# Kernel tuning notes

Hardware: AMD Instinct MI355X
Metric: run time of the kernel (lower is better)

Reference implementation:

```python
import jax, jax.numpy as jnp
import numpy as np

B = 512      # batch
H = 64       # latent_dim == GRU hidden size
F = 32       # n_features
S = 2048     # seq_len
NEG_SLOPE = 0.01  # nn.LeakyReLU default


def setup_inputs() -> dict:
    key = jax.random.key(0)
    ks = jax.random.split(key, 14)

    def p(k, shape, scale=0.1):
        return jax.random.normal(k, shape, dtype=jnp.float32) * scale

    return {
        "noise": jax.random.normal(ks[0], (B, H), dtype=jnp.float32),
        # GRU forward direction (layer 0): weight_ih_l0, weight_hh_l0, biases
        "W_ih_f": p(ks[1], (3 * H, H)),
        "W_hh_f": p(ks[2], (3 * H, H)),
        "b_ih_f": p(ks[3], (3 * H,)),
        "b_hh_f": p(ks[4], (3 * H,)),
        # GRU backward direction (layer 0 reverse)
        "W_ih_b": p(ks[5], (3 * H, H)),
        "W_hh_b": p(ks[6], (3 * H, H)),
        "b_ih_b": p(ks[7], (3 * H,)),
        "b_hh_b": p(ks[8], (3 * H,)),
        # latent_linear: Linear(2H -> H)
        "W_lat": p(ks[9], (H, 2 * H)),
        "b_lat": p(ks[10], (H,)),
        # output_linear: Linear(H -> F)
        "W_out": p(ks[11], (F, H)),
        "b_out": p(ks[12], (F,)),
    }


def _leaky(x):
    return jnp.where(x >= 0, x, NEG_SLOPE * x)


def _gru_cell(x, h, W_ih, W_hh, b_ih, b_hh):
    # PyTorch GRU cell: gates ordered (r, z, n)
    gi = x @ W_ih.T + b_ih          # (B, 3H)
    gh = h @ W_hh.T + b_hh          # (B, 3H)
    i_r, i_z, i_n = jnp.split(gi, 3, axis=-1)
    h_r, h_z, h_n = jnp.split(gh, 3, axis=-1)
    r = jax.nn.sigmoid(i_r + h_r)
    z = jax.nn.sigmoid(i_z + h_z)
    n = jnp.tanh(i_n + r * h_n)
    return (1.0 - z) * n + z * h


def reference(noise, W_ih_f, W_hh_f, b_ih_f, b_hh_f,
              W_ih_b, W_hh_b, b_ih_b, b_hh_b,
              W_lat, b_lat, W_out, b_out):
    # hidden_state = noise.repeat((D*n_layers,1,1)) -> both directions start at noise
    batch = noise.shape[0]

    def step(carry, _):
        x, hf, hb = carry
        # GRU on a length-1 sequence: each direction does one cell update;
        # output timestep = concat(fwd_out, bwd_out)
        hf2 = _gru_cell(x, hf, W_ih_f, W_hh_f, b_ih_f, b_hh_f)
        hb2 = _gru_cell(x, hb, W_ih_b, W_hh_b, b_ih_b, b_hh_b)
        out = jnp.concatenate([hf2, hb2], axis=-1)        # (B, 2H)
        lat = _leaky(out @ W_lat.T + b_lat)               # (B, H)
        return (lat, hf2, hb2), lat

    x0 = jnp.zeros((batch, H), dtype=noise.dtype)
    _, ys = jax.lax.scan(step, (x0, noise, noise), None, length=S)
    seq = jnp.transpose(ys, (1, 0, 2))   # (B, S, H)
    seq = _leaky(seq)                    # second LeakyReLU as in the original
    out = jax.nn.sigmoid(seq @ W_out.T + b_out)  # (B, S, F)
    return out
```

## Files before the change

kernel.cpp:

```cpp
#include <hip/hip_runtime.h>
#include <hip/hip_bf16.h>


#define NBATCH 512
#define NH 64
#define NS 2048
#define NF 32
#define MROW 16
#define LDH 72

typedef short s16x8 __attribute__((ext_vector_type(8)));
typedef float f32x4 __attribute__((ext_vector_type(4)));

#define MFMA(a, b, c) __builtin_amdgcn_mfma_f32_16x16x32_bf16((a), (b), (c), 0, 0, 0)

#define NLOG2E  (-1.4426950408889634f)
#define N2LOG2E (-2.8853900817779268f)

__device__ __forceinline__ short f2bf(float f) {
    return (short)((__float_as_uint(f) + 0x8000u) >> 16);
}

__device__ __forceinline__ f32x4 v_exp2(f32x4 a) {
    f32x4 r;
#pragma unroll
    for (int i = 0; i < 4; ++i) r[i] = __builtin_amdgcn_exp2f(a[i]);
    return r;
}

__device__ __forceinline__ f32x4 v_rcp(f32x4 a) {
    f32x4 r;
#pragma unroll
    for (int i = 0; i < 4; ++i) r[i] = __builtin_amdgcn_rcpf(a[i]);
    return r;
}

__device__ __forceinline__ f32x4 v_lk(f32x4 a) {
    f32x4 b = a * 0.01f;
    f32x4 r;
#pragma unroll
    for (int i = 0; i < 4; ++i) r[i] = fmaxf(a[i], b[i]);
    return r;
}

__device__ __forceinline__ f32x4 v_sigm(f32x4 a) {
    return v_rcp(v_exp2(a * NLOG2E) + 1.0f);
}

__device__ __forceinline__ int2 pk4bf(f32x4 v) {
    union { __hip_bfloat162 b; int i; } lo, hi;
    float2 a; a.x = v[0]; a.y = v[1];
    float2 b; b.x = v[2]; b.y = v[3];
    lo.b = __float22bfloat162_rn(a);
    hi.b = __float22bfloat162_rn(b);
    int2 r; r.x = lo.i; r.y = hi.i;
    return r;
}

__device__ __forceinline__ s16x8 bfragW(const float* __restrict__ W, int ldk,
                                        int row, int kf, int quad) {
    const float* p = W + (size_t)row * ldk + kf * 32 + quad * 8;
    s16x8 r;
#pragma unroll
    for (int i = 0; i < 8; ++i) r[i] = f2bf(p[i]);
    return r;
}

__device__ __forceinline__ f32x4 bias4(const float* __restrict__ p) {
    const float4 v = *(const float4*)p;
    f32x4 r = {v.x, v.y, v.z, v.w};
    return r;
}

__global__ __launch_bounds__(1024)
void grugan_kernel(const float* __restrict__ noise,
                   const float* __restrict__ Wihf, const float* __restrict__ Whhf,
                   const float* __restrict__ bihf, const float* __restrict__ bhhf,
                   const float* __restrict__ Wihb, const float* __restrict__ Whhb,
                   const float* __restrict__ bihb, const float* __restrict__ bhhb,
                   const float* __restrict__ Wlat, const float* __restrict__ blat,
                   const float* __restrict__ Wout, const float* __restrict__ bout,
                   float* __restrict__ out)
{
    __shared__ __align__(16) short Xs[2][MROW][LDH];
    __shared__ __align__(16) short X2s[2][MROW][LDH];
    __shared__ __align__(16) short Hs[2][2][MROW][LDH];

    const int tid  = threadIdx.x;
    const int wave = tid >> 6;
    const int lane = tid & 63;
    const int n    = lane & 15;
    const int quad = lane >> 4;
    const int row0 = blockIdx.x * MROW;

    for (int idx = tid; idx < MROW * LDH; idx += 1024) (&Xs[0][0][0])[idx] = 0;
    f32x4 hreg = {0.f, 0.f, 0.f, 0.f};
    const int gdir = wave >> 2;
    const int gjq  = (wave & 3) * 16 + quad * 4;
    if (wave < 8) {
        const float4 nz = *(const float4*)&noise[(size_t)(row0 + n) * NH + gjq];
        hreg[0] = nz.x; hreg[1] = nz.y; hreg[2] = nz.z; hreg[3] = nz.w;
        *(int2*)&Hs[0][gdir][n][gjq] = pk4bf(hreg);
    }
    __syncthreads();

    if (wave < 8) {
        const int dir  = gdir;
        const int cb   = wave & 3;
        const int jrow = cb * 16 + n;
        const int jq   = gjq;
        const float* Wih = dir ? Wihb : Wihf;
        const float* Whh = dir ? Whhb : Whhf;
        const float* bih = dir ? bihb : bihf;
        const float* bhh = dir ? bhhb : bhhf;

        s16x8 wir0 = bfragW(Wih, NH,   0 + jrow, 0, quad);
        s16x8 wir1 = bfragW(Wih, NH,   0 + jrow, 1, quad);
        s16x8 wiz0 = bfragW(Wih, NH,  64 + jrow, 0, quad);
        s16x8 wiz1 = bfragW(Wih, NH,  64 + jrow, 1, quad);
        s16x8 win0 = bfragW(Wih, NH, 128 + jrow, 0, quad);
        s16x8 win1 = bfragW(Wih, NH, 128 + jrow, 1, quad);
        s16x8 whr0 = bfragW(Whh, NH,   0 + jrow, 0, quad);
        s16x8 whr1 = bfragW(Whh, NH,   0 + jrow, 1, quad);
        s16x8 whz0 = bfragW(Whh, NH,  64 + jrow, 0, quad);
        s16x8 whz1 = bfragW(Whh, NH,  64 + jrow, 1, quad);
        s16x8 whn0 = bfragW(Whh, NH, 128 + jrow, 0, quad);
        s16x8 whn1 = bfragW(Whh, NH, 128 + jrow, 1, quad);
        f32x4 initR, initZ;
        {
            f32x4 a = bias4(&bih[jq]),      b = bias4(&bhh[jq]);
            initR = a + b;
            f32x4 c = bias4(&bih[64 + jq]), d = bias4(&bhh[64 + jq]);
            initZ = c + d;
        }
        const f32x4 initN1 = bias4(&bih[128 + jq]);
        const f32x4 initN2 = bias4(&bhh[128 + jq]);

        f32x4 accR, accZ, accN2;
        {
            s16x8 ha0 = *(const s16x8*)&Hs[0][dir][n][quad * 8];
            s16x8 ha1 = *(const s16x8*)&Hs[0][dir][n][32 + quad * 8];
            accR  = MFMA(whr0, ha0, initR);  accR  = MFMA(whr1, ha1, accR);
            accZ  = MFMA(whz0, ha0, initZ);  accZ  = MFMA(whz1, ha1, accZ);
            accN2 = MFMA(whn0, ha0, initN2); accN2 = MFMA(whn1, ha1, accN2);
        }

#define GSTEP(HB) do {                                                          \
        s16x8 xa0 = *(const s16x8*)&Xs[HB][n][quad * 8];                        \
        s16x8 xa1 = *(const s16x8*)&Xs[HB][n][32 + quad * 8];                   \
        accR = MFMA(wir0, xa0, accR);   accR = MFMA(wir1, xa1, accR);           \
        accZ = MFMA(wiz0, xa0, accZ);   accZ = MFMA(wiz1, xa1, accZ);           \
        f32x4 accN1 = MFMA(win0, xa0, initN1);                                  \
        accN1 = MFMA(win1, xa1, accN1);                                         \
        f32x4 eR = v_exp2(accR * NLOG2E);                                       \
        f32x4 rr = v_rcp(eR + 1.0f);                                            \
        f32x4 u  = accN1 + rr * accN2;                                          \
        f32x4 eU = v_exp2(u * N2LOG2E);                                         \
        f32x4 eZ = v_exp2(accZ * NLOG2E);                                       \
        f32x4 numer = (eZ + hreg) + eU * (hreg - eZ);                           \
        f32x4 denom = (eU + 1.0f) * (eZ + 1.0f);                                \
        hreg = numer * v_rcp(denom);                                            \
        *(int2*)&Hs[(HB) ^ 1][dir][n][jq] = pk4bf(hreg);                        \
        __syncthreads();                                \
        {                                                                       \
            s16x8 ha0 = *(const s16x8*)&Hs[(HB) ^ 1][dir][n][quad * 8];         \
            s16x8 ha1 = *(const s16x8*)&Hs[(HB) ^ 1][dir][n][32 + quad * 8];    \
            accR  = MFMA(whr0, ha0, initR);  accR  = MFMA(whr1, ha1, accR);     \
            accZ  = MFMA(whz0, ha0, initZ);  accZ  = MFMA(whz1, ha1, accZ);     \
            accN2 = MFMA(whn0, ha0, initN2); accN2 = MFMA(whn1, ha1, accN2);    \
        }                                                                       \
        __syncthreads();                                \
    } while (0)

        for (int t = 0; t < NS; t += 2) {
            GSTEP(0);
            GSTEP(1);
        }
#undef GSTEP
    } else if (wave < 12) {
        const int lt = wave & 3;
        const int nq = lt * 16 + quad * 4;
        s16x8 wl0 = bfragW(Wlat, 2 * NH, lt * 16 + n, 0, quad);
        s16x8 wl1 = bfragW(Wlat, 2 * NH, lt * 16 + n, 1, quad);
        s16x8 wl2 = bfragW(Wlat, 2 * NH, lt * 16 + n, 2, quad);
        s16x8 wl3 = bfragW(Wlat, 2 * NH, lt * 16 + n, 3, quad);
        const f32x4 initL = bias4(&blat[lt * 16 + quad * 4]);

#define LSTEP(HB) do {                                                          \
        __syncthreads();                                \
        s16x8 fa0 = *(const s16x8*)&Hs[(HB) ^ 1][0][n][quad * 8];               \
        s16x8 fa1 = *(const s16x8*)&Hs[(HB) ^ 1][0][n][32 + quad * 8];          \
        s16x8 ba0 = *(const s16x8*)&Hs[(HB) ^ 1][1][n][quad * 8];               \
        s16x8 ba1 = *(const s16x8*)&Hs[(HB) ^ 1][1][n][32 + quad * 8];          \
        f32x4 lac = MFMA(wl0, fa0, initL);                                      \
        lac = MFMA(wl1, fa1, lac);                                              \
        lac = MFMA(wl2, ba0, lac);                                              \
        lac = MFMA(wl3, ba1, lac);                                              \
        f32x4 la = v_lk(lac);                                                   \
        *(int2*)&Xs[(HB) ^ 1][n][nq]  = pk4bf(la);                              \
        *(int2*)&X2s[(HB) ^ 1][n][nq] = pk4bf(v_lk(la));                        \
        __syncthreads();                                \
    } while (0)

        for (int t = 0; t < NS; t += 2) {
            LSTEP(0);
            LSTEP(1);
        }
#undef LSTEP
    } else if (wave < 14) {
        const int f0 = (wave & 1) * 16;
        s16x8 wo0 = bfragW(Wout, NH, f0 + n, 0, quad);
        s16x8 wo1 = bfragW(Wout, NH, f0 + n, 1, quad);
        const f32x4 initO = bias4(&bout[f0 + quad * 4]);
        float* const orow = out + (size_t)(row0 + n) * (NS * NF) + f0 + quad * 4;
        f32x4 yv = {0.f, 0.f, 0.f, 0.f};

#define OSTEP(HB, T) do {                                                       \
        if ((T) >= 2)                                                           \
            *(f32x4*)(orow + (size_t)((T) - 2) * NF) = yv;                      \
        __syncthreads();                                                \
        if ((T) >= 1) {                                                         \
            s16x8 p0 = *(const s16x8*)&X2s[HB][n][quad * 8];                    \
            s16x8 p1 = *(const s16x8*)&X2s[HB][n][32 + quad * 8];               \
            f32x4 po = MFMA(wo0, p0, initO);                                    \
            po = MFMA(wo1, p1, po);                                             \
            yv = v_sigm(po);                                                    \
        }                                                                       \
        __syncthreads();                                                \
    } while (0)

        for (int t = 0; t < NS; t += 2) {
            OSTEP(0, t);
            OSTEP(1, t + 1);
        }
#undef OSTEP

        *(f32x4*)(orow + (size_t)(NS - 2) * NF) = yv;
        s16x8 p0 = *(const s16x8*)&X2s[0][n][quad * 8];
        s16x8 p1 = *(const s16x8*)&X2s[0][n][32 + quad * 8];
        f32x4 po = MFMA(wo0, p0, initO);
        po = MFMA(wo1, p1, po);
        *(f32x4*)(orow + (size_t)(NS - 1) * NF) = v_sigm(po);
    } else {
#pragma unroll 1
        for (int i = 0; i < 2 * NS; ++i) __syncthreads();
    }
}

extern "C" void kernel_launch(void* const* d_in, const int* in_sizes, int n_in,
                              void* d_out, int out_size, void* d_ws, size_t ws_size,
                              hipStream_t stream) {
    const float* noise = (const float*)d_in[0];
    const float* Wihf  = (const float*)d_in[1];
    const float* Whhf  = (const float*)d_in[2];
    const float* bihf  = (const float*)d_in[3];
    const float* bhhf  = (const float*)d_in[4];
    const float* Wihb  = (const float*)d_in[5];
    const float* Whhb  = (const float*)d_in[6];
    const float* bihb  = (const float*)d_in[7];
    const float* bhhb  = (const float*)d_in[8];
    const float* Wlat  = (const float*)d_in[9];
    const float* blat  = (const float*)d_in[10];
    const float* Wout  = (const float*)d_in[11];
    const float* bout  = (const float*)d_in[12];

    grugan_kernel<<<dim3(NBATCH / MROW), dim3(1024), 0, stream>>>(
        noise, Wihf, Whhf, bihf, bhhf, Wihb, Whhb, bihb, bhhb,
        Wlat, blat, Wout, bout, (float*)d_out);
}
```

Before: 1.613 ms.

## Merge output waves into latent waves and use non-draining raw barriers

The output projection moves into the two low latent waves, so the separate output waves and the idle barrier-only waves are dropped and the block shrinks from 1024 to 768 threads. The latent/output waves now use a raw s_barrier, and an s_barrier preceded only by an LDS wait, in place of __syncthreads. This keeps outstanding global stores of the output from stalling each per-timestep barrier. The latent MFMA chain is also split into two independent accumulators to shorten its dependency. The risk is a memory-ordering hazard if the hand-written barriers do not match the waits the compiler would otherwise insert, and the latent waves now sit longer on the serial critical path.

```diff
diff --git a/kernel.cpp b/kernel.cpp
--- a/kernel.cpp
+++ b/kernel.cpp
@@ -16,6 +16,14 @@
 
 #define NLOG2E  (-1.4426950408889634f)
 #define N2LOG2E (-2.8853900817779268f)
+
+__device__ __forceinline__ void bar_nodrain() {
+    asm volatile("s_barrier" ::: "memory");
+}
+
+__device__ __forceinline__ void bar_lgkm() {
+    asm volatile("s_waitcnt lgkmcnt(0)\n\ts_barrier" ::: "memory");
+}
 
 __device__ __forceinline__ short f2bf(float f) {
     return (short)((__float_as_uint(f) + 0x8000u) >> 16);
@@ -72,7 +80,7 @@
     return r;
 }
 
-__global__ __launch_bounds__(1024)
+__global__ __launch_bounds__(768)
 void grugan_kernel(const float* __restrict__ noise,
                    const float* __restrict__ Wihf, const float* __restrict__ Whhf,
                    const float* __restrict__ bihf, const float* __restrict__ bhhf,
@@ -93,7 +101,7 @@
     const int quad = lane >> 4;
     const int row0 = blockIdx.x * MROW;
 
-    for (int idx = tid; idx < MROW * LDH; idx += 1024) (&Xs[0][0][0])[idx] = 0;
+    for (int idx = tid; idx < MROW * LDH; idx += 768) (&Xs[0][0][0])[idx] = 0;
     f32x4 hreg = {0.f, 0.f, 0.f, 0.f};
     const int gdir = wave >> 2;
     const int gjq  = (wave & 3) * 16 + quad * 4;
@@ -177,7 +185,7 @@
             GSTEP(1);
         }
 #undef GSTEP
-    } else if (wave < 12) {
+    } else {
         const int lt = wave & 3;
         const int nq = lt * 16 + quad * 4;
         s16x8 wl0 = bfragW(Wlat, 2 * NH, lt * 16 + n, 0, quad);
@@ -186,64 +194,57 @@
         s16x8 wl3 = bfragW(Wlat, 2 * NH, lt * 16 + n, 3, quad);
         const f32x4 initL = bias4(&blat[lt * 16 + quad * 4]);
 
-#define LSTEP(HB) do {                                                          \
-        __syncthreads();                                \
+        s16x8 wo0 = {};
+        s16x8 wo1 = {};
+        f32x4 initO = {0.f, 0.f, 0.f, 0.f};
+        float* orow = nullptr;
+        if (lt < 2) {
+            const int f0 = lt * 16;
+            wo0   = bfragW(Wout, NH, f0 + n, 0, quad);
+            wo1   = bfragW(Wout, NH, f0 + n, 1, quad);
+            initO = bias4(&bout[f0 + quad * 4]);
+            orow  = out + (size_t)(row0 + n) * (NS * NF) + f0 + quad * 4;
+        }
+        const f32x4 zero4 = {0.f, 0.f, 0.f, 0.f};
+
+#define LOSTEP(HB, T) do {                                                      \
+        if (lt < 2 && (T) > 0) {                                                \
+                \
+                 \
+            s16x8 p0 = *(const s16x8*)&X2s[HB][n][quad * 8];                    \
+            s16x8 p1 = *(const s16x8*)&X2s[HB][n][32 + quad * 8];               \
+            f32x4 po = MFMA(wo0, p0, initO);                                    \
+            po = MFMA(wo1, p1, po);                                             \
+            *(f32x4*)(orow + (size_t)((T) - 1) * NF) = v_sigm(po);              \
+        }                                                                       \
+        bar_nodrain();        \
         s16x8 fa0 = *(const s16x8*)&Hs[(HB) ^ 1][0][n][quad * 8];               \
         s16x8 fa1 = *(const s16x8*)&Hs[(HB) ^ 1][0][n][32 + quad * 8];          \
         s16x8 ba0 = *(const s16x8*)&Hs[(HB) ^ 1][1][n][quad * 8];               \
         s16x8 ba1 = *(const s16x8*)&Hs[(HB) ^ 1][1][n][32 + quad * 8];          \
-        f32x4 lac = MFMA(wl0, fa0, initL);                                      \
-        lac = MFMA(wl1, fa1, lac);                                              \
-        lac = MFMA(wl2, ba0, lac);                                              \
-        lac = MFMA(wl3, ba1, lac);                                              \
-        f32x4 la = v_lk(lac);                                                   \
+        f32x4 lac1 = MFMA(wl0, fa0, initL);                                     \
+        lac1 = MFMA(wl1, fa1, lac1);                                            \
+        f32x4 lac2 = MFMA(wl2, ba0, zero4);                                     \
+        lac2 = MFMA(wl3, ba1, lac2);                                            \
+        f32x4 la = v_lk(lac1 + lac2);                                           \
         *(int2*)&Xs[(HB) ^ 1][n][nq]  = pk4bf(la);                              \
         *(int2*)&X2s[(HB) ^ 1][n][nq] = pk4bf(v_lk(la));                        \
-        __syncthreads();                                \
+        bar_lgkm();                   \
     } while (0)
 
         for (int t = 0; t < NS; t += 2) {
-            LSTEP(0);
-            LSTEP(1);
-        }
-#undef LSTEP
-    } else if (wave < 14) {
-        const int f0 = (wave & 1) * 16;
-        s16x8 wo0 = bfragW(Wout, NH, f0 + n, 0, quad);
-        s16x8 wo1 = bfragW(Wout, NH, f0 + n, 1, quad);
-        const f32x4 initO = bias4(&bout[f0 + quad * 4]);
-        float* const orow = out + (size_t)(row0 + n) * (NS * NF) + f0 + quad * 4;
-        f32x4 yv = {0.f, 0.f, 0.f, 0.f};
-
-#define OSTEP(HB, T) do {                                                       \
-        if ((T) >= 2)                                                           \
-            *(f32x4*)(orow + (size_t)((T) - 2) * NF) = yv;                      \
-        __syncthreads();                                                \
-        if ((T) >= 1) {                                                         \
-            s16x8 p0 = *(const s16x8*)&X2s[HB][n][quad * 8];                    \
-            s16x8 p1 = *(const s16x8*)&X2s[HB][n][32 + quad * 8];               \
-            f32x4 po = MFMA(wo0, p0, initO);                                    \
-            po = MFMA(wo1, p1, po);                                             \
-            yv = v_sigm(po);                                                    \
-        }                                                                       \
-        __syncthreads();                                                \
-    } while (0)
-
-        for (int t = 0; t < NS; t += 2) {
-            OSTEP(0, t);
-            OSTEP(1, t + 1);
-        }
-#undef OSTEP
-
-        *(f32x4*)(orow + (size_t)(NS - 2) * NF) = yv;
-        s16x8 p0 = *(const s16x8*)&X2s[0][n][quad * 8];
-        s16x8 p1 = *(const s16x8*)&X2s[0][n][32 + quad * 8];
-        f32x4 po = MFMA(wo0, p0, initO);
-        po = MFMA(wo1, p1, po);
-        *(f32x4*)(orow + (size_t)(NS - 1) * NF) = v_sigm(po);
-    } else {
-#pragma unroll 1
-        for (int i = 0; i < 2 * NS; ++i) __syncthreads();
+            LOSTEP(0, t);
+            LOSTEP(1, t + 1);
+        }
+#undef LOSTEP
+
+        if (lt < 2) {
+            s16x8 p0 = *(const s16x8*)&X2s[0][n][quad * 8];
+            s16x8 p1 = *(const s16x8*)&X2s[0][n][32 + quad * 8];
+            f32x4 po = MFMA(wo0, p0, initO);
+            po = MFMA(wo1, p1, po);
+            *(f32x4*)(orow + (size_t)(NS - 1) * NF) = v_sigm(po);
+        }
     }
 }
 
@@ -264,7 +265,7 @@
     const float* Wout  = (const float*)d_in[11];
     const float* bout  = (const float*)d_in[12];
 
-    grugan_kernel<<<dim3(NBATCH / MROW), dim3(1024), 0, stream>>>(
+    grugan_kernel<<<dim3(NBATCH / MROW), dim3(768), 0, stream>>>(
         noise, Wihf, Whhf, bihf, bhhf, Wihb, Whhb, bihb, bhhb,
         Wlat, blat, Wout, bout, (float*)d_out);
 }
```

Result: no change. 1.627 ms (+0.8%).
